# Kernel optimization log

Hardware: AMD Instinct MI355X
Metric: run time of the kernel (lower is better)

Reference implementation:

```python
import jax, jax.numpy as jnp
import numpy as np

N_NODES = 100000
N_EDGES = 1600000
D_IN = 128
D_HID = 128
N_CLASSES = 10


def setup_inputs() -> dict:
    key = jax.random.key(0)
    ks = jax.random.split(key, 9)
    x = jax.random.normal(ks[0], (N_NODES, D_IN), dtype=jnp.float32)
    edge_index = jax.random.randint(ks[1], (2, N_EDGES), 0, N_NODES, dtype=jnp.int64)
    edge_attr = jax.random.uniform(ks[2], (N_EDGES,), dtype=jnp.float32)
    s1 = 1.0 / np.sqrt(D_IN)
    s2 = 1.0 / np.sqrt(D_HID)
    W1 = jax.random.uniform(ks[3], (D_IN, D_HID), jnp.float32, -s1, s1)
    b1 = jnp.zeros((D_HID,), jnp.float32)
    W2 = jax.random.uniform(ks[4], (D_HID, D_HID), jnp.float32, -s2, s2)
    b2 = jnp.zeros((D_HID,), jnp.float32)
    Wm = jax.random.uniform(ks[5], (D_HID, N_CLASSES), jnp.float32, -s2, s2)
    bm = jax.random.uniform(ks[6], (N_CLASSES,), jnp.float32, -s2, s2)
    return {"x": x, "edge_index": edge_index, "edge_attr": edge_attr,
            "W1": W1, "b1": b1, "W2": W2, "b2": b2, "Wm": Wm, "bm": bm}


def _gcn_norm(edge_index, edge_attr, n_nodes):
    # PyG GCNConv default: add self-loops (weight 1), symmetric normalization.
    src, dst = edge_index[0], edge_index[1]
    loop = jnp.arange(n_nodes, dtype=src.dtype)
    src_f = jnp.concatenate([src, loop])
    dst_f = jnp.concatenate([dst, loop])
    w = jnp.concatenate([edge_attr, jnp.ones((n_nodes,), edge_attr.dtype)])
    deg = jax.ops.segment_sum(w, dst_f, num_segments=n_nodes)  # in-degree
    dinv = jnp.where(deg > 0, jax.lax.rsqrt(deg), 0.0)
    norm = dinv[src_f] * w * dinv[dst_f]  # [E + N]
    return src_f, dst_f, norm


def _gcn_conv(x, src_f, dst_f, norm, W, b, n_nodes):
    h = x @ W                                   # [N, D] dense transform first
    msg = h[src_f] * norm[:, None]              # gather + scale  [E+N, D]
    agg = jax.ops.segment_sum(msg, dst_f, num_segments=n_nodes)  # scatter-add
    return agg + b


def reference(x, edge_index, edge_attr, W1, b1, W2, b2, Wm, bm):
    n = x.shape[0]
    src_f, dst_f, norm = _gcn_norm(edge_index, edge_attr, n)
    h = jax.nn.relu(_gcn_conv(x, src_f, dst_f, norm, W1, b1, n))
    h = jax.nn.relu(_gcn_conv(h, src_f, dst_f, norm, W2, b2, n))
    # F.dropout(training=False) is identity in eval mode
    pooled = jnp.mean(h, axis=0)                # global mean pool -> [D_HID]
    return pooled @ Wm + bm                     # [N_CLASSES]
```

## Files before the change

### kernel.cpp

```cpp
#include <hip/hip_runtime.h>

#define N_NODES_C 100000
#define N_EDGES_C 1600000
#define D_C 128
#define N_CLASSES_C 10
#define POOL_BLOCKS_C 2048
#define POOL2_C 128
#define NBUCKET 391
#define BUCKET_CAP 4608
#define BPAD 16
#define EPB 4096
#define NB_A ((N_EDGES_C + EPB - 1) / EPB)

using bf16x8 = __attribute__((ext_vector_type(8))) short;
using f32x4  = __attribute__((ext_vector_type(4))) float;

__device__ __forceinline__ unsigned int pack_bf2(float a, float b) {
    unsigned int ua = __float_as_uint(a);
    unsigned int ub = __float_as_uint(b);
    ua = (ua + 0x7FFFu + ((ua >> 16) & 1u)) >> 16;
    ub = (ub + 0x7FFFu + ((ub >> 16) & 1u)) & 0xFFFF0000u;
    return ua | ub;
}

__device__ __forceinline__ void bf8_fma(uint4 r, float v, float* acc) {
    acc[0] = fmaf(v, __uint_as_float(r.x << 16), acc[0]);
    acc[1] = fmaf(v, __uint_as_float(r.x & 0xFFFF0000u), acc[1]);
    acc[2] = fmaf(v, __uint_as_float(r.y << 16), acc[2]);
    acc[3] = fmaf(v, __uint_as_float(r.y & 0xFFFF0000u), acc[3]);
    acc[4] = fmaf(v, __uint_as_float(r.z << 16), acc[4]);
    acc[5] = fmaf(v, __uint_as_float(r.z & 0xFFFF0000u), acc[5]);
    acc[6] = fmaf(v, __uint_as_float(r.w << 16), acc[6]);
    acc[7] = fmaf(v, __uint_as_float(r.w & 0xFFFF0000u), acc[7]);
}

__device__ __forceinline__ int edge_word(const int* __restrict__ ei, long long idx, int is64) {
    return is64 ? ei[2 * idx] : ei[idx];
}

__global__ void detect_init_kernel(const int* __restrict__ ei, int* __restrict__ flag,
                                   int* __restrict__ bcnt) {
    int t = threadIdx.x;
    if (blockIdx.x == 0) {
        if (t < 64) {
            int nz = 0;
            for (int i = t; i < 512; i += 64) nz |= ei[2 * i + 1];
            unsigned long long b = __ballot(nz != 0);
            if (t == 0) *flag = (b == 0ULL) ? 1 : 0;
        }
    } else {
        int i = (blockIdx.x - 1) * 256 + t;
        if (i < NBUCKET * BPAD) bcnt[i] = 0;
    }
}

__global__ __launch_bounds__(512) void bucket_fill_kernel(
        const int* __restrict__ ei, const float* __restrict__ attr,
        const int* __restrict__ flag, int* __restrict__ bcnt, int2* __restrict__ bkt) {
    __shared__ int2 stage[EPB];
    __shared__ unsigned short sbin[EPB];
    __shared__ int hist[512];
    __shared__ int lstart[512];
    __shared__ int cursor[NBUCKET];
    __shared__ int gbase[NBUCKET];

    const int t = threadIdx.x;
    const long long e0 = (long long)blockIdx.x * EPB;
    const int n = (N_EDGES_C - e0 < EPB) ? (int)(N_EDGES_C - e0) : EPB;
    const int is64 = *flag;

    hist[t] = 0;
    __syncthreads();

    int  myb[8];
    int2 myrec[8];
#pragma unroll
    for (int j = 0; j < 8; ++j) {
        int i = t + j * 512;
        myb[j] = -1;
        if (i < n) {
            long long e = e0 + i;
            int s = edge_word(ei, e, is64);
            int d = edge_word(ei, (long long)N_EDGES_C + e, is64);
            float a = attr[e];
            int b = d >> 8;
            myb[j] = b;
            myrec[j].x = s | ((d & 0xFF) << 17);
            myrec[j].y = __float_as_int(a);
            atomicAdd(&hist[b], 1);
        }
    }
    __syncthreads();

    const int myh = hist[t];
    lstart[t] = myh;
    __syncthreads();
    for (int off = 1; off < 512; off <<= 1) {
        int v = lstart[t];
        int add = (t >= off) ? lstart[t - off] : 0;
        __syncthreads();
        lstart[t] = v + add;
        __syncthreads();
    }
    int excl = lstart[t] - myh;
    if (t < NBUCKET) cursor[t] = excl;
    lstart[t] = excl;
    __syncthreads();

#pragma unroll
    for (int j = 0; j < 8; ++j) {
        if (myb[j] >= 0) {
            int slot = atomicAdd(&cursor[myb[j]], 1);
            stage[slot] = myrec[j];
            sbin[slot] = (unsigned short)myb[j];
        }
    }
    if (t < NBUCKET) {
        int k = myh;
        gbase[t] = k ? atomicAdd(&bcnt[t * BPAD], k) : 0;
    }
    __syncthreads();

    for (int i = t; i < n; i += 512) {
        int b = sbin[i];
        int local = gbase[b] + (i - lstart[b]);
        if (local < BUCKET_CAP)
            bkt[(long long)b * BUCKET_CAP + local] = stage[i];
    }
}

__global__ __launch_bounds__(256) void bucket_sort_kernel(
        const int* __restrict__ bcnt, int2* __restrict__ bkt,
        int2* __restrict__ rowinfo, float* __restrict__ dinv) {
    __shared__ int2 recA[BUCKET_CAP];
    __shared__ int2 recB[BUCKET_CAP];
    __shared__ int hist[256], lstart[256], cursor[256];
    __shared__ float degs[256];

    const int b = blockIdx.x, t = threadIdx.x;
    int n = bcnt[b * BPAD];
    if (n > BUCKET_CAP) n = BUCKET_CAP;
    int2* win = bkt + (long long)b * BUCKET_CAP;

    hist[t] = 0;
    degs[t] = 0.f;
    __syncthreads();

    for (int i = t; i < n; i += 256) {
        int2 cv = win[i];
        recA[i] = cv;
        int d = (cv.x >> 17) & 0xFF;
        atomicAdd(&hist[d], 1);
        atomicAdd(&degs[d], __int_as_float(cv.y));
    }
    __syncthreads();

    const int myh = hist[t];
    lstart[t] = myh;
    __syncthreads();
    for (int off = 1; off < 256; off <<= 1) {
        int v = lstart[t];
        int add = (t >= off) ? lstart[t - off] : 0;
        __syncthreads();
        lstart[t] = v + add;
        __syncthreads();
    }
    int excl = lstart[t] - myh;
    cursor[t] = excl;
    lstart[t] = excl;
    __syncthreads();

    for (int i = t; i < n; i += 256) {
        int2 cv = recA[i];
        int d = (cv.x >> 17) & 0xFF;
        int slot = atomicAdd(&cursor[d], 1);
        int2 o;
        o.x = cv.x & 0x1FFFF;
        o.y = cv.y;
        recB[slot] = o;
    }
    __syncthreads();

    for (int i = t; i < n; i += 256) win[i] = recB[i];

    int node = b * 256 + t;
    if (node < N_NODES_C) {
        int2 ri;
        ri.x = b * BUCKET_CAP + lstart[t];
        ri.y = myh;
        rowinfo[node] = ri;
        dinv[node] = rsqrtf(1.0f + degs[t]);
    }
}

__global__ __launch_bounds__(256) void prep_w_kernel(const float* __restrict__ W1,
                                                     const float* __restrict__ W2,
                                                     unsigned short* __restrict__ Wp1,
                                                     unsigned short* __restrict__ Wp2) {
    const float* W = (blockIdx.x & 8) ? W2 : W1;
    unsigned short* Wp = (blockIdx.x & 8) ? Wp2 : Wp1;
    const int n = blockIdx.x & 7;
    const int t = threadIdx.x;
    const int s = t >> 6, l = t & 63;
    const int col = n * 16 + (l & 15);
    const int k0 = s * 32 + (l >> 4) * 8;
    float v[8];
#pragma unroll
    for (int j = 0; j < 8; ++j) v[j] = W[(k0 + j) * 128 + col];
    uint4 o;
    o.x = pack_bf2(v[0], v[1]);
    o.y = pack_bf2(v[2], v[3]);
    o.z = pack_bf2(v[4], v[5]);
    o.w = pack_bf2(v[6], v[7]);
    ((uint4*)Wp)[(n * 4 + s) * 64 + l] = o;
}

template <bool AF32>
__global__ __launch_bounds__(256) void gemm_mfma(const void* __restrict__ A,
                                                 const unsigned short* __restrict__ Wp,
                                                 const float* __restrict__ dinv,
                                                 unsigned short* __restrict__ H,
                                                 int nrows) {
    __shared__ unsigned short Bl[2048 * 8];
    {
        const uint4* src = (const uint4*)Wp;
        uint4* dst = (uint4*)Bl;
        for (int i = threadIdx.x; i < 2048; i += 256) dst[i] = src[i];
    }
    __syncthreads();

    const int wid = threadIdx.x >> 6, lane = threadIdx.x & 63;
    const int rowA = lane & 15, kg = lane >> 4;
    const int r0 = blockIdx.x * 128 + wid * 32;

    bf16x8 afr[2][4];
#pragma unroll
    for (int m = 0; m < 2; ++m) {
        int row = r0 + m * 16 + rowA;
        if (row >= nrows) row = nrows - 1;
        if constexpr (AF32) {
            const float* xp = (const float*)A + (long long)row * D_C + kg * 8;
#pragma unroll
            for (int s = 0; s < 4; ++s) {
                float4 lo = *(const float4*)(xp + s * 32);
                float4 hi = *(const float4*)(xp + s * 32 + 4);
                uint4 pk;
                pk.x = pack_bf2(lo.x, lo.y);
                pk.y = pack_bf2(lo.z, lo.w);
                pk.z = pack_bf2(hi.x, hi.y);
                pk.w = pack_bf2(hi.z, hi.w);
                afr[m][s] = __builtin_bit_cast(bf16x8, pk);
            }
        } else {
            const unsigned short* xp = (const unsigned short*)A + (long long)row * D_C + kg * 8;
#pragma unroll
            for (int s = 0; s < 4; ++s) afr[m][s] = *(const bf16x8*)(xp + s * 32);
        }
    }

    f32x4 acc[2][8];
#pragma unroll
    for (int m = 0; m < 2; ++m)
#pragma unroll
        for (int n = 0; n < 8; ++n) acc[m][n] = (f32x4){0.f, 0.f, 0.f, 0.f};

#pragma unroll
    for (int n = 0; n < 8; ++n) {
#pragma unroll
        for (int s = 0; s < 4; ++s) {
            bf16x8 bfr = *(const bf16x8*)(Bl + ((n * 4 + s) * 64 + lane) * 8);
            acc[0][n] = __builtin_amdgcn_mfma_f32_16x16x32_bf16(afr[0][s], bfr, acc[0][n], 0, 0, 0);
            acc[1][n] = __builtin_amdgcn_mfma_f32_16x16x32_bf16(afr[1][s], bfr, acc[1][n], 0, 0, 0);
        }
    }

    const int colb = lane & 15, rq = lane >> 4;
#pragma unroll
    for (int m = 0; m < 2; ++m) {
#pragma unroll
        for (int q = 0; q < 4; ++q) {
            int row = r0 + m * 16 + rq * 4 + q;
            if (row >= nrows) continue;
            float sc = dinv[row];
#pragma unroll
            for (int n = 0; n < 8; ++n) {
                unsigned int u = __float_as_uint(acc[m][n][q] * sc);
                u = (u + 0x7FFFu + ((u >> 16) & 1u)) >> 16;
                H[(long long)row * D_C + n * 16 + colb] = (unsigned short)u;
            }
        }
    }
}

template <int MODE>
__global__ __launch_bounds__(256) void agg_kernel(
        const unsigned short* __restrict__ h, const float* __restrict__ dinv,
        const int2* __restrict__ rowinfo, const int2* __restrict__ recs,
        const float* __restrict__ bias, void* __restrict__ out_v) {
    __shared__ float pool[128];
    if (MODE == 1) {
        if (threadIdx.x < 128) pool[threadIdx.x] = 0.f;
        __syncthreads();
    }
    const int g    = threadIdx.x >> 4;
    const int sub  = threadIdx.x & 15;
    const int lane = threadIdx.x & 63;
    const int grp  = lane >> 4;

    const float4 bA = *(const float4*)(bias + sub * 8);
    const float4 bB = *(const float4*)(bias + sub * 8 + 4);
    float p[8] = {0.f, 0.f, 0.f, 0.f, 0.f, 0.f, 0.f, 0.f};

    for (int i = blockIdx.x * 16 + g; i < N_NODES_C; i += gridDim.x * 16) {
        const float di = dinv[i];
        const int2 ri = rowinfo[i];
        const int2* row = recs + ri.x;
        const int m = ri.y;

        float acc[8] = {0.f, 0.f, 0.f, 0.f, 0.f, 0.f, 0.f, 0.f};
        {
            uint4 r = *(const uint4*)(h + (long long)i * D_C + sub * 8);
            bf8_fma(r, 1.0f, acc);
        }
        int j = 0;
        for (; j + 7 < m; j += 8) {
            int2 c0 = row[j + 0], c1 = row[j + 1], c2 = row[j + 2], c3 = row[j + 3];
            int2 c4 = row[j + 4], c5 = row[j + 5], c6 = row[j + 6], c7 = row[j + 7];
            uint4 r0 = *(const uint4*)(h + (long long)c0.x * D_C + sub * 8);
            uint4 r1 = *(const uint4*)(h + (long long)c1.x * D_C + sub * 8);
            uint4 r2 = *(const uint4*)(h + (long long)c2.x * D_C + sub * 8);
            uint4 r3 = *(const uint4*)(h + (long long)c3.x * D_C + sub * 8);
            uint4 r4 = *(const uint4*)(h + (long long)c4.x * D_C + sub * 8);
            uint4 r5 = *(const uint4*)(h + (long long)c5.x * D_C + sub * 8);
            uint4 r6 = *(const uint4*)(h + (long long)c6.x * D_C + sub * 8);
            uint4 r7 = *(const uint4*)(h + (long long)c7.x * D_C + sub * 8);
            bf8_fma(r0, __int_as_float(c0.y), acc);
            bf8_fma(r1, __int_as_float(c1.y), acc);
            bf8_fma(r2, __int_as_float(c2.y), acc);
            bf8_fma(r3, __int_as_float(c3.y), acc);
            bf8_fma(r4, __int_as_float(c4.y), acc);
            bf8_fma(r5, __int_as_float(c5.y), acc);
            bf8_fma(r6, __int_as_float(c6.y), acc);
            bf8_fma(r7, __int_as_float(c7.y), acc);
        }
        for (; j + 3 < m; j += 4) {
            int2 c0 = row[j + 0], c1 = row[j + 1], c2 = row[j + 2], c3 = row[j + 3];
            uint4 r0 = *(const uint4*)(h + (long long)c0.x * D_C + sub * 8);
            uint4 r1 = *(const uint4*)(h + (long long)c1.x * D_C + sub * 8);
            uint4 r2 = *(const uint4*)(h + (long long)c2.x * D_C + sub * 8);
            uint4 r3 = *(const uint4*)(h + (long long)c3.x * D_C + sub * 8);
            bf8_fma(r0, __int_as_float(c0.y), acc);
            bf8_fma(r1, __int_as_float(c1.y), acc);
            bf8_fma(r2, __int_as_float(c2.y), acc);
            bf8_fma(r3, __int_as_float(c3.y), acc);
        }
        for (; j < m; ++j) {
            int2 cv = row[j];
            uint4 r = *(const uint4*)(h + (long long)cv.x * D_C + sub * 8);
            bf8_fma(r, __int_as_float(cv.y), acc);
        }

        float o[8];
        o[0] = fmaxf(fmaf(acc[0], di, bA.x), 0.f);
        o[1] = fmaxf(fmaf(acc[1], di, bA.y), 0.f);
        o[2] = fmaxf(fmaf(acc[2], di, bA.z), 0.f);
        o[3] = fmaxf(fmaf(acc[3], di, bA.w), 0.f);
        o[4] = fmaxf(fmaf(acc[4], di, bB.x), 0.f);
        o[5] = fmaxf(fmaf(acc[5], di, bB.y), 0.f);
        o[6] = fmaxf(fmaf(acc[6], di, bB.z), 0.f);
        o[7] = fmaxf(fmaf(acc[7], di, bB.w), 0.f);

        if (MODE == 0) {
            uint4 pk;
            pk.x = pack_bf2(o[0], o[1]);
            pk.y = pack_bf2(o[2], o[3]);
            pk.z = pack_bf2(o[4], o[5]);
            pk.w = pack_bf2(o[6], o[7]);
            *(uint4*)((unsigned short*)out_v + (long long)i * D_C + sub * 8) = pk;
        } else {
#pragma unroll
            for (int k = 0; k < 8; ++k) p[k] += o[k];
        }
    }

    if (MODE == 1) {
#pragma unroll
        for (int k = 0; k < 8; ++k) {
            p[k] += __shfl_xor(p[k], 16);
            p[k] += __shfl_xor(p[k], 32);
        }
        if (grp == 0) {
#pragma unroll
            for (int k = 0; k < 8; ++k) atomicAdd(&pool[sub * 8 + k], p[k]);
        }
        __syncthreads();
        if (threadIdx.x < 128)
            ((float*)out_v)[blockIdx.x * 128 + threadIdx.x] = pool[threadIdx.x];
    }
}

__global__ __launch_bounds__(256) void reduce_part_kernel(const float* __restrict__ part,
                                                          float* __restrict__ part2) {
    __shared__ float tmp[128];
    const int f = threadIdx.x & 127;
    const int half = threadIdx.x >> 7;
    const int r0 = blockIdx.x * 16 + half * 8;
    float s = 0.f;
#pragma unroll
    for (int r = 0; r < 8; ++r) s += part[(r0 + r) * 128 + f];
    if (half == 0) tmp[f] = s;
    __syncthreads();
    if (half == 1) part2[blockIdx.x * 128 + f] = tmp[f] + s;
}

__global__ __launch_bounds__(1024) void final_kernel(const float* __restrict__ part2,
                                                     const float* __restrict__ Wm,
                                                     const float* __restrict__ bm,
                                                     float* __restrict__ out) {
    __shared__ float red[8][128];
    __shared__ float pooled[128];
    int t = threadIdx.x;
    int f = t & 127, c = t >> 7;
    float s = 0.f;
    for (int b = c; b < POOL2_C; b += 8) s += part2[b * 128 + f];
    red[c][f] = s;
    __syncthreads();
    if (t < 128) {
        float tot = 0.f;
#pragma unroll
        for (int cc = 0; cc < 8; ++cc) tot += red[cc][t];
        pooled[t] = tot / (float)N_NODES_C;
    }
    __syncthreads();
    if (t < N_CLASSES_C) {
        float o = bm[t];
        for (int ff = 0; ff < 128; ++ff) o = fmaf(pooled[ff], Wm[ff * N_CLASSES_C + t], o);
        out[t] = o;
    }
}

extern "C" void kernel_launch(void* const* d_in, const int* in_sizes, int n_in,
                              void* d_out, int out_size, void* d_ws, size_t ws_size,
                              hipStream_t stream) {
    const float* x    = (const float*)d_in[0];
    const int*   ei   = (const int*)d_in[1];
    const float* attr = (const float*)d_in[2];
    const float* W1   = (const float*)d_in[3];
    const float* b1   = (const float*)d_in[4];
    const float* W2   = (const float*)d_in[5];
    const float* b2   = (const float*)d_in[6];
    const float* Wm   = (const float*)d_in[7];
    const float* bm   = (const float*)d_in[8];
    float* out = (float*)d_out;

    char* ws = (char*)d_ws;
    size_t off = 0;
    auto alloc = [&](size_t bytes) -> char* {
        char* p = ws + off;
        off += (bytes + 255) & ~(size_t)255;
        return p;
    };
    int*            flag    = (int*)alloc(4);
    int*            bcnt    = (int*)alloc((size_t)NBUCKET * BPAD * 4);
    int2*           rowinfo = (int2*)alloc((size_t)N_NODES_C * 8);
    float*          dinv    = (float*)alloc((size_t)N_NODES_C * 4);
    int2*           bkt     = (int2*)alloc((size_t)NBUCKET * BUCKET_CAP * 8);
    float*          part    = (float*)alloc((size_t)POOL_BLOCKS_C * 128 * 4);
    float*          part2   = (float*)alloc((size_t)POOL2_C * 128 * 4);
    unsigned short* Wp1     = (unsigned short*)alloc(2048 * 8 * 2);
    unsigned short* Wp2     = (unsigned short*)alloc(2048 * 8 * 2);
    unsigned short* hbuf    = (unsigned short*)alloc((size_t)N_NODES_C * D_C * 2);
    unsigned short* hb2     = (unsigned short*)alloc((size_t)N_NODES_C * D_C * 2);
    (void)ws_size;

    const int ntiles = (N_NODES_C + 127) / 128;
    const int agg_blocks = (N_NODES_C + 15) / 16;
    const int init_blocks = 1 + (NBUCKET * BPAD + 255) / 256;

    detect_init_kernel<<<init_blocks, 256, 0, stream>>>(ei, flag, bcnt);
    bucket_fill_kernel<<<NB_A, 512, 0, stream>>>(ei, attr, flag, bcnt, bkt);
    bucket_sort_kernel<<<NBUCKET, 256, 0, stream>>>(bcnt, bkt, rowinfo, dinv);
    prep_w_kernel<<<16, 256, 0, stream>>>(W1, W2, Wp1, Wp2);

    gemm_mfma<true><<<ntiles, 256, 0, stream>>>(x, Wp1, dinv, hbuf, N_NODES_C);
    agg_kernel<0><<<agg_blocks, 256, 0, stream>>>(hbuf, dinv, rowinfo, bkt, b1, hb2);
    gemm_mfma<false><<<ntiles, 256, 0, stream>>>(hb2, Wp2, dinv, hbuf, N_NODES_C);
    agg_kernel<1><<<POOL_BLOCKS_C, 256, 0, stream>>>(hbuf, dinv, rowinfo, bkt, b2, part);
    reduce_part_kernel<<<POOL2_C, 256, 0, stream>>>(part, part2);
    final_kernel<<<1, 1024, 0, stream>>>(part2, Wm, bm, out);
}
```

Before: 217.5 us.

## Drop LDS staging in bucket kernels and merge weight prep into setup

Folds the weight bf16 packing kernel into the init/detect kernel, which saves one launch. bucket_fill no longer stages and locally sorts records in shared memory. Instead it reserves global offsets per bucket and scatters each record directly. bucket_sort keeps its records in a per-thread register array instead of two large LDS buffers, replaces the LDS scan with a wave shuffle scan, and writes the sorted output in place. This greatly cuts LDS use and barrier count, which should raise occupancy. The trade-off is less coalesced global writes, and the dynamically indexed register array may spill to scratch.

```diff
diff --git a/kernel.cpp b/kernel.cpp
--- a/kernel.cpp
+++ b/kernel.cpp
@@ -38,9 +38,12 @@
     return is64 ? ei[2 * idx] : ei[idx];
 }
 
-__global__ void detect_init_kernel(const int* __restrict__ ei, int* __restrict__ flag,
-                                   int* __restrict__ bcnt) {
-    int t = threadIdx.x;
+__global__ __launch_bounds__(256) void setup_kernel(
+        const int* __restrict__ ei, const float* __restrict__ W1,
+        const float* __restrict__ W2, int* __restrict__ flag,
+        int* __restrict__ bcnt, unsigned short* __restrict__ Wp1,
+        unsigned short* __restrict__ Wp2) {
+    const int t = threadIdx.x;
     if (blockIdx.x == 0) {
         if (t < 64) {
             int nz = 0;
@@ -48,19 +51,33 @@
             unsigned long long b = __ballot(nz != 0);
             if (t == 0) *flag = (b == 0ULL) ? 1 : 0;
         }
-    } else {
+    } else if (blockIdx.x < 26) {
         int i = (blockIdx.x - 1) * 256 + t;
         if (i < NBUCKET * BPAD) bcnt[i] = 0;
+    } else {
+        const int pb = blockIdx.x - 26;
+        const float* W = (pb & 8) ? W2 : W1;
+        unsigned short* Wp = (pb & 8) ? Wp2 : Wp1;
+        const int n = pb & 7;
+        const int s = t >> 6, l = t & 63;
+        const int col = n * 16 + (l & 15);
+        const int k0 = s * 32 + (l >> 4) * 8;
+        float v[8];
+#pragma unroll
+        for (int j = 0; j < 8; ++j) v[j] = W[(k0 + j) * 128 + col];
+        uint4 o;
+        o.x = pack_bf2(v[0], v[1]);
+        o.y = pack_bf2(v[2], v[3]);
+        o.z = pack_bf2(v[4], v[5]);
+        o.w = pack_bf2(v[6], v[7]);
+        ((uint4*)Wp)[(n * 4 + s) * 64 + l] = o;
     }
 }
 
 __global__ __launch_bounds__(512) void bucket_fill_kernel(
         const int* __restrict__ ei, const float* __restrict__ attr,
         const int* __restrict__ flag, int* __restrict__ bcnt, int2* __restrict__ bkt) {
-    __shared__ int2 stage[EPB];
-    __shared__ unsigned short sbin[EPB];
-    __shared__ int hist[512];
-    __shared__ int lstart[512];
+    __shared__ int hist[NBUCKET];
     __shared__ int cursor[NBUCKET];
     __shared__ int gbase[NBUCKET];
 
@@ -69,7 +86,7 @@
     const int n = (N_EDGES_C - e0 < EPB) ? (int)(N_EDGES_C - e0) : EPB;
     const int is64 = *flag;
 
-    hist[t] = 0;
+    for (int i = t; i < NBUCKET; i += 512) hist[i] = 0;
     __syncthreads();
 
     int  myb[8];
@@ -83,59 +100,38 @@
             int s = edge_word(ei, e, is64);
             int d = edge_word(ei, (long long)N_EDGES_C + e, is64);
             float a = attr[e];
-            int b = d >> 8;
-            myb[j] = b;
+            myb[j] = d >> 8;
             myrec[j].x = s | ((d & 0xFF) << 17);
             myrec[j].y = __float_as_int(a);
-            atomicAdd(&hist[b], 1);
-        }
-    }
-    __syncthreads();
-
-    const int myh = hist[t];
-    lstart[t] = myh;
-    __syncthreads();
-    for (int off = 1; off < 512; off <<= 1) {
-        int v = lstart[t];
-        int add = (t >= off) ? lstart[t - off] : 0;
-        __syncthreads();
-        lstart[t] = v + add;
-        __syncthreads();
-    }
-    int excl = lstart[t] - myh;
-    if (t < NBUCKET) cursor[t] = excl;
-    lstart[t] = excl;
+            atomicAdd(&hist[myb[j]], 1);
+        }
+    }
+    __syncthreads();
+
+    for (int i = t; i < NBUCKET; i += 512) {
+        int k = hist[i];
+        gbase[i] = k ? atomicAdd(&bcnt[i * BPAD], k) : 0;
+        cursor[i] = 0;
+    }
     __syncthreads();
 
 #pragma unroll
     for (int j = 0; j < 8; ++j) {
         if (myb[j] >= 0) {
-            int slot = atomicAdd(&cursor[myb[j]], 1);
-            stage[slot] = myrec[j];
-            sbin[slot] = (unsigned short)myb[j];
-        }
-    }
-    if (t < NBUCKET) {
-        int k = myh;
-        gbase[t] = k ? atomicAdd(&bcnt[t * BPAD], k) : 0;
-    }
-    __syncthreads();
-
-    for (int i = t; i < n; i += 512) {
-        int b = sbin[i];
-        int local = gbase[b] + (i - lstart[b]);
-        if (local < BUCKET_CAP)
-            bkt[(long long)b * BUCKET_CAP + local] = stage[i];
+            int b = myb[j];
+            int r = gbase[b] + atomicAdd(&cursor[b], 1);
+            if (r < BUCKET_CAP)
+                bkt[(long long)b * BUCKET_CAP + r] = myrec[j];
+        }
     }
 }
 
 __global__ __launch_bounds__(256) void bucket_sort_kernel(
         const int* __restrict__ bcnt, int2* __restrict__ bkt,
         int2* __restrict__ rowinfo, float* __restrict__ dinv) {
-    __shared__ int2 recA[BUCKET_CAP];
-    __shared__ int2 recB[BUCKET_CAP];
     __shared__ int hist[256], lstart[256], cursor[256];
     __shared__ float degs[256];
+    __shared__ int wsum[4];
 
     const int b = blockIdx.x, t = threadIdx.x;
     int n = bcnt[b * BPAD];
@@ -146,9 +142,11 @@
     degs[t] = 0.f;
     __syncthreads();
 
+    int2 rec[18];
+    int nk = 0;
     for (int i = t; i < n; i += 256) {
         int2 cv = win[i];
-        recA[i] = cv;
+        rec[nk++] = cv;
         int d = (cv.x >> 17) & 0xFF;
         atomicAdd(&hist[d], 1);
         atomicAdd(&degs[d], __int_as_float(cv.y));
@@ -156,32 +154,30 @@
     __syncthreads();
 
     const int myh = hist[t];
-    lstart[t] = myh;
-    __syncthreads();
-    for (int off = 1; off < 256; off <<= 1) {
-        int v = lstart[t];
-        int add = (t >= off) ? lstart[t - off] : 0;
-        __syncthreads();
-        lstart[t] = v + add;
-        __syncthreads();
-    }
-    int excl = lstart[t] - myh;
+    int v = myh;
+#pragma unroll
+    for (int off = 1; off < 64; off <<= 1) {
+        int u = __shfl_up(v, off);
+        if ((t & 63) >= off) v += u;
+    }
+    if ((t & 63) == 63) wsum[t >> 6] = v;
+    __syncthreads();
+    int woff = 0;
+    for (int w = 0; w < (t >> 6); ++w) woff += wsum[w];
+    const int excl = woff + v - myh;
     cursor[t] = excl;
     lstart[t] = excl;
     __syncthreads();
 
-    for (int i = t; i < n; i += 256) {
-        int2 cv = recA[i];
+    for (int k = 0; k < nk; ++k) {
+        int2 cv = rec[k];
         int d = (cv.x >> 17) & 0xFF;
         int slot = atomicAdd(&cursor[d], 1);
         int2 o;
         o.x = cv.x & 0x1FFFF;
         o.y = cv.y;
-        recB[slot] = o;
-    }
-    __syncthreads();
-
-    for (int i = t; i < n; i += 256) win[i] = recB[i];
+        win[slot] = o;
+    }
 
     int node = b * 256 + t;
     if (node < N_NODES_C) {
@@ -191,28 +187,6 @@
         rowinfo[node] = ri;
         dinv[node] = rsqrtf(1.0f + degs[t]);
     }
-}
-
-__global__ __launch_bounds__(256) void prep_w_kernel(const float* __restrict__ W1,
-                                                     const float* __restrict__ W2,
-                                                     unsigned short* __restrict__ Wp1,
-                                                     unsigned short* __restrict__ Wp2) {
-    const float* W = (blockIdx.x & 8) ? W2 : W1;
-    unsigned short* Wp = (blockIdx.x & 8) ? Wp2 : Wp1;
-    const int n = blockIdx.x & 7;
-    const int t = threadIdx.x;
-    const int s = t >> 6, l = t & 63;
-    const int col = n * 16 + (l & 15);
-    const int k0 = s * 32 + (l >> 4) * 8;
-    float v[8];
-#pragma unroll
-    for (int j = 0; j < 8; ++j) v[j] = W[(k0 + j) * 128 + col];
-    uint4 o;
-    o.x = pack_bf2(v[0], v[1]);
-    o.y = pack_bf2(v[2], v[3]);
-    o.z = pack_bf2(v[4], v[5]);
-    o.w = pack_bf2(v[6], v[7]);
-    ((uint4*)Wp)[(n * 4 + s) * 64 + l] = o;
 }
 
 template <bool AF32>
@@ -475,12 +449,10 @@
 
     const int ntiles = (N_NODES_C + 127) / 128;
     const int agg_blocks = (N_NODES_C + 15) / 16;
-    const int init_blocks = 1 + (NBUCKET * BPAD + 255) / 256;
-
-    detect_init_kernel<<<init_blocks, 256, 0, stream>>>(ei, flag, bcnt);
+
+    setup_kernel<<<42, 256, 0, stream>>>(ei, W1, W2, flag, bcnt, Wp1, Wp2);
     bucket_fill_kernel<<<NB_A, 512, 0, stream>>>(ei, attr, flag, bcnt, bkt);
     bucket_sort_kernel<<<NBUCKET, 256, 0, stream>>>(bcnt, bkt, rowinfo, dinv);
-    prep_w_kernel<<<16, 256, 0, stream>>>(W1, W2, Wp1, Wp2);
 
     gemm_mfma<true><<<ntiles, 256, 0, stream>>>(x, Wp1, dinv, hbuf, N_NODES_C);
     agg_kernel<0><<<agg_blocks, 256, 0, stream>>>(hbuf, dinv, rowinfo, bkt, b1, hb2);
```

Measured after the change: 223.8 us. 2.9% more time.
